# Performance work log

Measured on AMD Instinct MI355X. Metric: run time of the kernel, lower is better.

## Reference

```python
import jax, jax.numpy as jnp
import numpy as np

N_EMBD = 1024
HEAD_SIZE = 128

def setup_inputs() -> dict:
    key = jax.random.key(0)
    k1, k2, k3, k4 = jax.random.split(key, 4)
    x = jax.random.normal(k1, (8, 2048, N_EMBD), dtype=jnp.float32)
    # Linear(n_embd, head_size, bias=False): y = x @ W, W: [n_embd, head_size]
    s = 1.0 / np.sqrt(N_EMBD)
    Wk = jax.random.uniform(k2, (N_EMBD, HEAD_SIZE), jnp.float32, -s, s)
    Wq = jax.random.uniform(k3, (N_EMBD, HEAD_SIZE), jnp.float32, -s, s)
    Wv = jax.random.uniform(k4, (N_EMBD, HEAD_SIZE), jnp.float32, -s, s)
    return {"x": x, "Wk": Wk, "Wq": Wq, "Wv": Wv}

def reference(x, Wk, Wq, Wv):
    B, T, C = x.shape
    H = Wk.shape[1]
    k = jnp.einsum('btc,ch->bth', x, Wk)
    q = jnp.einsum('btc,ch->bth', x, Wq)
    v = jnp.einsum('btc,ch->bth', x, Wv)
    # scores [B, T, T], causal mask, scaled by head_size**-0.5
    wei = jnp.einsum('bqh,bkh->bqk', q, k) * (H ** -0.5)
    causal = jnp.tril(jnp.ones((T, T), dtype=bool))
    wei = jnp.where(causal, wei, -jnp.inf)
    wei = jax.nn.softmax(wei, axis=-1)
    # dropout p=0.0 (eval mode): identity
    out = jnp.einsum('bqk,bkh->bqh', wei, v)
    return out
```

## Files before the change

### kernel.cpp

```cpp
#include <hip/hip_runtime.h>
#include <hip/hip_bf16.h>
#include <stdint.h>

typedef short v8s __attribute__((ext_vector_type(8)));
typedef float v4f __attribute__((ext_vector_type(4)));
typedef float v16f __attribute__((ext_vector_type(16)));

#define N_EMBD 1024
#define HEAD 128
#define TOKENS 16384
#define T_SEQ 2048
#define BATCH 8
#define BPB 96

__device__ __forceinline__ short f2bf(float f) {
    union { float f; uint32_t u; } c; c.f = f;
    uint32_t u = c.u;
    uint32_t r = (u + 0x7fffu + ((u >> 16) & 1u)) >> 16;
    return (short)r;
}

__device__ __forceinline__ float bf2f(short s) {
    union { uint32_t u; float f; } c; c.u = ((uint32_t)(uint16_t)s) << 16;
    return c.f;
}

__global__ __launch_bounds__(256)
void wt_kernel(const float* __restrict__ Wq, const float* __restrict__ Wk,
               const float* __restrict__ Wv, short* __restrict__ wpk) {
    int tid = blockIdx.x * 256 + threadIdx.x;
    int w   = tid >> 17;
    int rem = tid & 131071;
    int c = rem >> 7, h = rem & 127;
    const float* src = (w == 0) ? Wq : ((w == 1) ? Wk : Wv);
    int cb = h >> 5, kb = c >> 4;
    int l  = (h & 31) | (((c >> 3) & 1) << 5);
    wpk[((((w * 4 + cb) * 64) + kb) * 64 + l) * 8 + (c & 7)] = f2bf(src[rem]);
}

__global__ __launch_bounds__(256)
void xpk_kernel(const float* __restrict__ x, short* __restrict__ xpk) {
    const int rb = blockIdx.x >> 1;
    const int kh = blockIdx.x & 1;
    const int t  = threadIdx.x;

    __shared__ short sX[32 * 520];

    for (int it = 0; it < 8; ++it) {
        int idx = it * 256 + t;
        int tok = idx >> 6, ko = idx & 63;
        const float* src = x + (size_t)(rb * 32 + tok) * 1024 + kh * 512 + ko * 8;
        float4 lo = *(const float4*)(src);
        float4 hi = *(const float4*)(src + 4);
        union { short s[8]; uint4 u; } p;
        p.s[0] = f2bf(lo.x); p.s[1] = f2bf(lo.y); p.s[2] = f2bf(lo.z); p.s[3] = f2bf(lo.w);
        p.s[4] = f2bf(hi.x); p.s[5] = f2bf(hi.y); p.s[6] = f2bf(hi.z); p.s[7] = f2bf(hi.w);
        *(uint4*)(&sX[tok * 520 + ko * 8]) = p.u;
    }
    __syncthreads();

    for (int it = 0; it < 8; ++it) {
        int kb_loc = it * 4 + (t >> 6);
        int l = t & 63;
        uint4 d = *(const uint4*)(&sX[(l & 31) * 520 + kb_loc * 16 + (l >> 5) * 8]);
        int kb = kh * 32 + kb_loc;
        *(uint4*)(&xpk[(((size_t)rb * 64 + kb) * 64 + l) * 8]) = d;
    }
}

__global__ __launch_bounds__(256)
void qkv_gemm(const short* __restrict__ xpk, const short* __restrict__ wpk,
              short* __restrict__ qkv, short* __restrict__ vT) {
    const int bid = blockIdx.x;
    const int xcd = bid & 7, q = bid >> 3;
    const int mt  = xcd * 32 + q / 3;
    const int w   = q % 3;
    const int m0  = mt * 64;

    __shared__ short sT[128 * 72];

    const int t = threadIdx.x;
    const int lane = t & 63, wv = t >> 6;
    const int l31 = lane & 31, l1 = lane >> 5;
    const int wm = wv & 1, wn = wv >> 1;

    const int rb = mt * 2 + wm;
    const short* ap  = xpk + (size_t)rb * 32768 + lane * 8;
    const short* bp0 = wpk + (size_t)(w * 4 + 2 * wn) * 32768 + lane * 8;
    const short* bp1 = wpk + (size_t)(w * 4 + 2 * wn + 1) * 32768 + lane * 8;

    v16f acc[2];
    for (int i = 0; i < 16; ++i) { acc[0][i] = 0.f; acc[1][i] = 0.f; }

    v8s A0k0, A0k1, A1k0, A1k1;
    v8s B0k0n0, B0k0n1, B0k1n0, B0k1n1, B1k0n0, B1k0n1, B1k1n0, B1k1n1;

#define LOADSET0(IT) do { int o_ = (IT) * 1024;                                  \
        A0k0   = *(const v8s*)(ap  + o_);                                        \
        A0k1   = *(const v8s*)(ap  + o_ + 512);                                  \
        B0k0n0 = *(const v8s*)(bp0 + o_);                                        \
        B0k0n1 = *(const v8s*)(bp1 + o_);                                        \
        B0k1n0 = *(const v8s*)(bp0 + o_ + 512);                                  \
        B0k1n1 = *(const v8s*)(bp1 + o_ + 512);                                  \
    } while (0)

#define LOADSET1(IT) do { int o_ = (IT) * 1024;                                  \
        A1k0   = *(const v8s*)(ap  + o_);                                        \
        A1k1   = *(const v8s*)(ap  + o_ + 512);                                  \
        B1k0n0 = *(const v8s*)(bp0 + o_);                                        \
        B1k0n1 = *(const v8s*)(bp1 + o_);                                        \
        B1k1n0 = *(const v8s*)(bp0 + o_ + 512);                                  \
        B1k1n1 = *(const v8s*)(bp1 + o_ + 512);                                  \
    } while (0)

#define COMPUTE0() do {                                                          \
        acc[0] = __builtin_amdgcn_mfma_f32_32x32x16_bf16(A0k0, B0k0n0, acc[0], 0, 0, 0); \
        acc[1] = __builtin_amdgcn_mfma_f32_32x32x16_bf16(A0k0, B0k0n1, acc[1], 0, 0, 0); \
        acc[0] = __builtin_amdgcn_mfma_f32_32x32x16_bf16(A0k1, B0k1n0, acc[0], 0, 0, 0); \
        acc[1] = __builtin_amdgcn_mfma_f32_32x32x16_bf16(A0k1, B0k1n1, acc[1], 0, 0, 0); \
    } while (0)

#define COMPUTE1() do {                                                          \
        acc[0] = __builtin_amdgcn_mfma_f32_32x32x16_bf16(A1k0, B1k0n0, acc[0], 0, 0, 0); \
        acc[1] = __builtin_amdgcn_mfma_f32_32x32x16_bf16(A1k0, B1k0n1, acc[1], 0, 0, 0); \
        acc[0] = __builtin_amdgcn_mfma_f32_32x32x16_bf16(A1k1, B1k1n0, acc[0], 0, 0, 0); \
        acc[1] = __builtin_amdgcn_mfma_f32_32x32x16_bf16(A1k1, B1k1n1, acc[1], 0, 0, 0); \
    } while (0)

    LOADSET0(0);
    LOADSET1(1);
    for (int it = 0; it < 32; it += 2) {
        COMPUTE0();
        if (it + 2 < 32) LOADSET0(it + 2);
        COMPUTE1();
        if (it + 3 < 32) LOADSET1(it + 3);
    }

#undef LOADSET0
#undef LOADSET1
#undef COMPUTE0
#undef COMPUTE1

    if (w < 2) {
        short* outw = qkv + (size_t)w * TOKENS * HEAD;
        for (int ni = 0; ni < 2; ++ni) {
            int col = wn * 64 + ni * 32 + l31;
            for (int reg = 0; reg < 16; ++reg) {
                int m = (reg & 3) + 8 * (reg >> 2) + 4 * l1;
                outw[(size_t)(m0 + wm * 32 + m) * HEAD + col] = f2bf(acc[ni][reg]);
            }
        }
    } else {
        __syncthreads();
        for (int ni = 0; ni < 2; ++ni) {
            int col = wn * 64 + ni * 32 + l31;
            for (int g = 0; g < 4; ++g) {
                union { short s[4]; uint64_t u; } pk;
                for (int r = 0; r < 4; ++r) pk.s[r] = f2bf(acc[ni][g * 4 + r]);
                *(uint64_t*)(&sT[col * 72 + wm * 32 + 8 * g + 4 * l1]) = pk.u;
            }
        }
        __syncthreads();
        for (int it = 0; it < 4; ++it) {
            int c = it * 256 + t;
            int col = c >> 3, c8 = c & 7;
            uint4 d = *(const uint4*)(&sT[col * 72 + c8 * 8]);
            *(uint4*)(&vT[(size_t)col * TOKENS + m0 + c8 * 8]) = d;
        }
    }
}

__global__ __launch_bounds__(256)
void attn_kernel(const short* __restrict__ qb, const short* __restrict__ kb,
                 const short* __restrict__ vT, short* __restrict__ po,
                 float* __restrict__ pl) {
    const int bid = blockIdx.x;
    const int b  = bid & 7;
    const int r0 = bid >> 3;
    int qt2 = 0, c0 = 0;
    for (;;) { int sz = (2 * qt2 + 4) / 3; if (r0 < c0 + sz) break; c0 += sz; ++qt2; }
    const int s = r0 - c0;
    const int q0 = qt2 * 128;
    const int nkt = 2 * qt2 + 2;
    const int kt0 = s * 3;
    const int kt1 = (kt0 + 3 < nkt) ? (kt0 + 3) : nkt;

    __shared__ short sK[64 * 128];
    __shared__ short sV[128 * 64];
    __shared__ short sP[128 * 72];

    const int t = threadIdx.x;
    const int wv = t >> 6, lane = t & 63, ln = lane & 15, qd = lane >> 4;
    const int wrow0 = q0 + wv * 32;

    v8s qf[2][4];
    for (int qg = 0; qg < 2; ++qg) {
        const short* qrow = qb + ((size_t)(b * T_SEQ + wrow0 + qg * 16 + ln)) * HEAD;
        for (int ks = 0; ks < 4; ++ks)
            qf[qg][ks] = *(const v8s*)(qrow + ks * 32 + qd * 8);
    }

    v4f o[2][8] = {};
    float rs[2] = {0.f, 0.f};
    const float sc = 1.4426950408889634f / 11.313708498984761f;

    for (int kt = kt0; kt < kt1; ++kt) {
        __syncthreads();
        const short* kbase = kb + ((size_t)(b * T_SEQ + kt * 64)) * HEAD;
        for (int it = 0; it < 4; ++it) {
            int c = it * 256 + t;
            int row = c >> 4, ch = c & 15;
            uint4 d = *(const uint4*)(kbase + row * HEAD + ch * 8);
            int sch = (ch & 8) | ((ch ^ row) & 7);
            *(uint4*)(&sK[row * 128 + sch * 8]) = d;
        }
        const short* vbase = vT + (size_t)(b * T_SEQ + kt * 64);
        for (int it = 0; it < 4; ++it) {
            int c = it * 256 + t;
            int dd = c >> 3, ch = c & 7;
            uint4 d = *(const uint4*)(vbase + (size_t)dd * TOKENS + ch * 8);
            *(uint4*)(&sV[dd * 64 + ((ch ^ dd) & 7) * 8]) = d;
        }
        __syncthreads();

        if (kt * 64 >= wrow0 + 32) continue;

        v4f st[2][4] = {};
        for (int ni = 0; ni < 4; ++ni) {
            int krow = ni * 16 + ln;
            for (int ks = 0; ks < 4; ++ks) {
                int ch = ks * 4 + qd;
                v8s kf = *(const v8s*)&sK[krow * 128 + ((ch & 8) | ((ch ^ krow) & 7)) * 8];
                st[0][ni] = __builtin_amdgcn_mfma_f32_16x16x32_bf16(kf, qf[0][ks], st[0][ni], 0, 0, 0);
                st[1][ni] = __builtin_amdgcn_mfma_f32_16x16x32_bf16(kf, qf[1][ks], st[1][ni], 0, 0, 0);
            }
        }

        const bool needMask = (kt * 64 + 63 > wrow0);
        for (int qg = 0; qg < 2; ++qg) {
            int prow = wv * 32 + qg * 16 + ln;
            int qrow_g = wrow0 + qg * 16 + ln;
            for (int ni = 0; ni < 4; ++ni) {
                union { short s[4]; uint64_t u; } pk;
                for (int r = 0; r < 4; ++r) {
                    float p = exp2f(st[qg][ni][r] * sc);
                    int kg = kt * 64 + ni * 16 + qd * 4 + r;
                    if (needMask && kg > qrow_g) p = 0.f;
                    rs[qg] += p;
                    pk.s[r] = f2bf(p);
                }
                *(uint64_t*)(&sP[prow * 72 + ni * 16 + qd * 4]) = pk.u;
            }
        }

        for (int kk2 = 0; kk2 < 2; ++kk2) {
            v8s pf0 = *(const v8s*)&sP[(wv * 32 + ln) * 72 + kk2 * 32 + qd * 8];
            v8s pf1 = *(const v8s*)&sP[(wv * 32 + 16 + ln) * 72 + kk2 * 32 + qd * 8];
            for (int oni = 0; oni < 8; ++oni) {
                int dd = oni * 16 + ln;
                int ch = kk2 * 4 + qd;
                v8s vf = *(const v8s*)&sV[dd * 64 + ((ch ^ dd) & 7) * 8];
                o[0][oni] = __builtin_amdgcn_mfma_f32_16x16x32_bf16(vf, pf0, o[0][oni], 0, 0, 0);
                o[1][oni] = __builtin_amdgcn_mfma_f32_16x16x32_bf16(vf, pf1, o[1][oni], 0, 0, 0);
            }
        }
    }

    float lsum[2];
    for (int qg = 0; qg < 2; ++qg) {
        float v = rs[qg];
        v += __shfl_xor(v, 16);
        v += __shfl_xor(v, 32);
        lsum[qg] = v;
    }

    short* pob = po + (size_t)bid * 128 * 128;
    for (int qg = 0; qg < 2; ++qg)
        for (int oni = 0; oni < 8; ++oni) {
            union { short s[4]; uint2 u; } pk;
            for (int r = 0; r < 4; ++r) pk.s[r] = f2bf(o[qg][oni][r]);
            *(uint2*)(&pob[(((qg * 8 + oni) * 4 + wv) * 64 + lane) * 4]) = pk.u;
        }
    if (lane < 16)
        for (int qg = 0; qg < 2; ++qg)
            pl[bid * 128 + wv * 32 + qg * 16 + lane] = lsum[qg];
}

__global__ __launch_bounds__(256)
void combine_kernel(const short* __restrict__ po, const float* __restrict__ pl,
                    float* __restrict__ out) {
    const int bid = blockIdx.x;
    const int dh  = bid & 1;
    const int qh  = (bid >> 1) & 1;
    const int qt2 = (bid >> 2) & 15;
    const int b   = bid >> 6;
    int cum = 0;
    for (int j = 0; j < qt2; ++j) cum += (2 * j + 4) / 3;
    const int S = (2 * qt2 + 4) / 3;

    const int t = threadIdx.x;
    const int wv = t >> 6, lane = t & 63, ln = lane & 15, qd = lane >> 4;

    float l = 0.f;
    float accv[4][4] = {};

    for (int si = 0; si < S; ++si) {
        int slot = (cum + si) * 8 + b;
        l += pl[slot * 128 + wv * 32 + qh * 16 + ln];
        const short* pob = po + (size_t)slot * 16384;
        for (int oi = 0; oi < 4; ++oi) {
            int oni = dh * 4 + oi;
            union { short s[4]; uint2 u; } pk;
            pk.u = *(const uint2*)(&pob[(((qh * 8 + oni) * 4 + wv) * 64 + lane) * 4]);
            for (int r = 0; r < 4; ++r) accv[oi][r] += bf2f(pk.s[r]);
        }
    }
    float inv = 1.f / l;
    float* ob = out + ((size_t)(b * T_SEQ) + qt2 * 128 + wv * 32 + qh * 16 + ln) * HEAD;
    for (int oi = 0; oi < 4; ++oi) {
        float4 o4 = make_float4(accv[oi][0] * inv, accv[oi][1] * inv,
                                accv[oi][2] * inv, accv[oi][3] * inv);
        *(float4*)(ob + (dh * 4 + oi) * 16 + qd * 4) = o4;
    }
}

extern "C" void kernel_launch(void* const* d_in, const int* in_sizes, int n_in,
                              void* d_out, int out_size, void* d_ws, size_t ws_size,
                              hipStream_t stream) {
    const float* x  = (const float*)d_in[0];
    const float* Wk = (const float*)d_in[1];
    const float* Wq = (const float*)d_in[2];
    const float* Wv = (const float*)d_in[3];
    float* out = (float*)d_out;

    char* ws = (char*)d_ws;
    short* wpk = (short*)ws;
    short* xpk = (short*)(ws + 0x100000u);
    short* qb  = (short*)(ws + 0x2100000u);
    short* kb  = (short*)(ws + 0x2500000u);
    short* vT  = (short*)(ws + 0x2900000u);
    short* po  = (short*)ws;
    float* pl  = (float*)(ws + 0x1800000u);
    short* qkv = qb;

    wt_kernel<<<1536, 256, 0, stream>>>(Wq, Wk, Wv, wpk);
    xpk_kernel<<<1024, 256, 0, stream>>>(x, xpk);
    qkv_gemm<<<768, 256, 0, stream>>>(xpk, wpk, qkv, vT);
    attn_kernel<<<BATCH * BPB, 256, 0, stream>>>(qb, kb, vT, po, pl);
    combine_kernel<<<512, 256, 0, stream>>>(po, pl, out);
}
```

Before: 166.5 us.

## Pre-pack K and V into MFMA fragment layout and read directly from global

The QKV GEMM epilogue now writes K and V tiles already arranged in the per-lane MFMA operand layout, staging them through shared memory. The attention kernel then drops its shared-memory staging of K and V and its two block barriers per key tile, loading operand fragments straight from global memory with coalesced 16-byte loads. It also exits the key loop early once tiles are fully masked. The trade-off is that each of the four waves reloads the same K/V fragments from global/L2, with no LDS reuse, so latency is exposed without explicit prefetch.

```diff
diff --git a/kernel.cpp b/kernel.cpp
--- a/kernel.cpp
+++ b/kernel.cpp
@@ -70,7 +70,8 @@
 
 __global__ __launch_bounds__(256)
 void qkv_gemm(const short* __restrict__ xpk, const short* __restrict__ wpk,
-              short* __restrict__ qkv, short* __restrict__ vT) {
+              short* __restrict__ qkv, short* __restrict__ kpk,
+              short* __restrict__ vpk) {
     const int bid = blockIdx.x;
     const int xcd = bid & 7, q = bid >> 3;
     const int mt  = xcd * 32 + q / 3;
@@ -141,17 +142,34 @@
 #undef COMPUTE0
 #undef COMPUTE1
 
-    if (w < 2) {
-        short* outw = qkv + (size_t)w * TOKENS * HEAD;
+    const int b_  = m0 >> 11;
+    const int kt_ = (m0 >> 6) & 31;
+    if (w == 0) {
         for (int ni = 0; ni < 2; ++ni) {
             int col = wn * 64 + ni * 32 + l31;
             for (int reg = 0; reg < 16; ++reg) {
                 int m = (reg & 3) + 8 * (reg >> 2) + 4 * l1;
-                outw[(size_t)(m0 + wm * 32 + m) * HEAD + col] = f2bf(acc[ni][reg]);
+                qkv[(size_t)(m0 + wm * 32 + m) * HEAD + col] = f2bf(acc[ni][reg]);
             }
         }
+    } else if (w == 1) {
+        for (int ni = 0; ni < 2; ++ni) {
+            int col = wn * 64 + ni * 32 + l31;
+            for (int reg = 0; reg < 16; ++reg) {
+                int m = (reg & 3) + 8 * (reg >> 2) + 4 * l1;
+                sT[(wm * 32 + m) * 136 + col] = f2bf(acc[ni][reg]);
+            }
+        }
+        __syncthreads();
+        short* kdst = kpk + ((size_t)(b_ * 32 + kt_) * 16) * 512;
+        for (int it = 0; it < 4; ++it) {
+            int c = it * 256 + t;
+            int chunk = c >> 6, l = c & 63;
+            int ni2 = chunk >> 2, ks = chunk & 3;
+            uint4 d = *(const uint4*)(&sT[(ni2 * 16 + (l & 15)) * 136 + ks * 32 + (l >> 4) * 8]);
+            *(uint4*)(&kdst[chunk * 512 + l * 8]) = d;
+        }
     } else {
-        __syncthreads();
         for (int ni = 0; ni < 2; ++ni) {
             int col = wn * 64 + ni * 32 + l31;
             for (int g = 0; g < 4; ++g) {
@@ -161,18 +179,20 @@
             }
         }
         __syncthreads();
+        short* vdst = vpk + ((size_t)(b_ * 32 + kt_) * 16) * 512;
         for (int it = 0; it < 4; ++it) {
             int c = it * 256 + t;
-            int col = c >> 3, c8 = c & 7;
-            uint4 d = *(const uint4*)(&sT[col * 72 + c8 * 8]);
-            *(uint4*)(&vT[(size_t)col * TOKENS + m0 + c8 * 8]) = d;
-        }
-    }
-}
-
-__global__ __launch_bounds__(256)
-void attn_kernel(const short* __restrict__ qb, const short* __restrict__ kb,
-                 const short* __restrict__ vT, short* __restrict__ po,
+            int chunk = c >> 6, l = c & 63;
+            int oni = chunk >> 1, kk2 = chunk & 1;
+            uint4 d = *(const uint4*)(&sT[(oni * 16 + (l & 15)) * 72 + kk2 * 32 + (l >> 4) * 8]);
+            *(uint4*)(&vdst[chunk * 512 + l * 8]) = d;
+        }
+    }
+}
+
+__global__ __launch_bounds__(256)
+void attn_kernel(const short* __restrict__ qb, const short* __restrict__ kpk,
+                 const short* __restrict__ vpk, short* __restrict__ po,
                  float* __restrict__ pl) {
     const int bid = blockIdx.x;
     const int b  = bid & 7;
@@ -185,8 +205,6 @@
     const int kt0 = s * 3;
     const int kt1 = (kt0 + 3 < nkt) ? (kt0 + 3) : nkt;
 
-    __shared__ short sK[64 * 128];
-    __shared__ short sV[128 * 64];
     __shared__ short sP[128 * 72];
 
     const int t = threadIdx.x;
@@ -204,36 +222,29 @@
     float rs[2] = {0.f, 0.f};
     const float sc = 1.4426950408889634f / 11.313708498984761f;
 
+    const short* kbB = kpk + ((size_t)b * 32 * 16) * 512 + lane * 8;
+    const short* vbB = vpk + ((size_t)b * 32 * 16) * 512 + lane * 8;
+
     for (int kt = kt0; kt < kt1; ++kt) {
-        __syncthreads();
-        const short* kbase = kb + ((size_t)(b * T_SEQ + kt * 64)) * HEAD;
-        for (int it = 0; it < 4; ++it) {
-            int c = it * 256 + t;
-            int row = c >> 4, ch = c & 15;
-            uint4 d = *(const uint4*)(kbase + row * HEAD + ch * 8);
-            int sch = (ch & 8) | ((ch ^ row) & 7);
-            *(uint4*)(&sK[row * 128 + sch * 8]) = d;
-        }
-        const short* vbase = vT + (size_t)(b * T_SEQ + kt * 64);
-        for (int it = 0; it < 4; ++it) {
-            int c = it * 256 + t;
-            int dd = c >> 3, ch = c & 7;
-            uint4 d = *(const uint4*)(vbase + (size_t)dd * TOKENS + ch * 8);
-            *(uint4*)(&sV[dd * 64 + ((ch ^ dd) & 7) * 8]) = d;
-        }
-        __syncthreads();
-
-        if (kt * 64 >= wrow0 + 32) continue;
+        if (kt * 64 >= wrow0 + 32) break;
+        const short* kc = kbB + (size_t)kt * 8192;
+        const short* vc = vbB + (size_t)kt * 8192;
 
         v4f st[2][4] = {};
+#pragma unroll
         for (int ni = 0; ni < 4; ++ni) {
-            int krow = ni * 16 + ln;
-            for (int ks = 0; ks < 4; ++ks) {
-                int ch = ks * 4 + qd;
-                v8s kf = *(const v8s*)&sK[krow * 128 + ((ch & 8) | ((ch ^ krow) & 7)) * 8];
-                st[0][ni] = __builtin_amdgcn_mfma_f32_16x16x32_bf16(kf, qf[0][ks], st[0][ni], 0, 0, 0);
-                st[1][ni] = __builtin_amdgcn_mfma_f32_16x16x32_bf16(kf, qf[1][ks], st[1][ni], 0, 0, 0);
-            }
+            v8s kf0 = *(const v8s*)(kc + (ni * 4 + 0) * 512);
+            v8s kf1 = *(const v8s*)(kc + (ni * 4 + 1) * 512);
+            v8s kf2 = *(const v8s*)(kc + (ni * 4 + 2) * 512);
+            v8s kf3 = *(const v8s*)(kc + (ni * 4 + 3) * 512);
+            st[0][ni] = __builtin_amdgcn_mfma_f32_16x16x32_bf16(kf0, qf[0][0], st[0][ni], 0, 0, 0);
+            st[1][ni] = __builtin_amdgcn_mfma_f32_16x16x32_bf16(kf0, qf[1][0], st[1][ni], 0, 0, 0);
+            st[0][ni] = __builtin_amdgcn_mfma_f32_16x16x32_bf16(kf1, qf[0][1], st[0][ni], 0, 0, 0);
+            st[1][ni] = __builtin_amdgcn_mfma_f32_16x16x32_bf16(kf1, qf[1][1], st[1][ni], 0, 0, 0);
+            st[0][ni] = __builtin_amdgcn_mfma_f32_16x16x32_bf16(kf2, qf[0][2], st[0][ni], 0, 0, 0);
+            st[1][ni] = __builtin_amdgcn_mfma_f32_16x16x32_bf16(kf2, qf[1][2], st[1][ni], 0, 0, 0);
+            st[0][ni] = __builtin_amdgcn_mfma_f32_16x16x32_bf16(kf3, qf[0][3], st[0][ni], 0, 0, 0);
+            st[1][ni] = __builtin_amdgcn_mfma_f32_16x16x32_bf16(kf3, qf[1][3], st[1][ni], 0, 0, 0);
         }
 
         const bool needMask = (kt * 64 + 63 > wrow0);
@@ -253,16 +264,27 @@
             }
         }
 
-        for (int kk2 = 0; kk2 < 2; ++kk2) {
-            v8s pf0 = *(const v8s*)&sP[(wv * 32 + ln) * 72 + kk2 * 32 + qd * 8];
-            v8s pf1 = *(const v8s*)&sP[(wv * 32 + 16 + ln) * 72 + kk2 * 32 + qd * 8];
-            for (int oni = 0; oni < 8; ++oni) {
-                int dd = oni * 16 + ln;
-                int ch = kk2 * 4 + qd;
-                v8s vf = *(const v8s*)&sV[dd * 64 + ((ch ^ dd) & 7) * 8];
-                o[0][oni] = __builtin_amdgcn_mfma_f32_16x16x32_bf16(vf, pf0, o[0][oni], 0, 0, 0);
-                o[1][oni] = __builtin_amdgcn_mfma_f32_16x16x32_bf16(vf, pf1, o[1][oni], 0, 0, 0);
-            }
+        v8s pf[2][2];
+#pragma unroll
+        for (int qg = 0; qg < 2; ++qg)
+#pragma unroll
+            for (int kk2 = 0; kk2 < 2; ++kk2)
+                pf[qg][kk2] = *(const v8s*)&sP[(wv * 32 + qg * 16 + ln) * 72 + kk2 * 32 + qd * 8];
+
+#pragma unroll
+        for (int og = 0; og < 4; ++og) {
+            v8s vf00 = *(const v8s*)(vc + ((og * 2 + 0) * 2 + 0) * 512);
+            v8s vf01 = *(const v8s*)(vc + ((og * 2 + 0) * 2 + 1) * 512);
+            v8s vf10 = *(const v8s*)(vc + ((og * 2 + 1) * 2 + 0) * 512);
+            v8s vf11 = *(const v8s*)(vc + ((og * 2 + 1) * 2 + 1) * 512);
+            o[0][og * 2]     = __builtin_amdgcn_mfma_f32_16x16x32_bf16(vf00, pf[0][0], o[0][og * 2], 0, 0, 0);
+            o[0][og * 2]     = __builtin_amdgcn_mfma_f32_16x16x32_bf16(vf01, pf[0][1], o[0][og * 2], 0, 0, 0);
+            o[1][og * 2]     = __builtin_amdgcn_mfma_f32_16x16x32_bf16(vf00, pf[1][0], o[1][og * 2], 0, 0, 0);
+            o[1][og * 2]     = __builtin_amdgcn_mfma_f32_16x16x32_bf16(vf01, pf[1][1], o[1][og * 2], 0, 0, 0);
+            o[0][og * 2 + 1] = __builtin_amdgcn_mfma_f32_16x16x32_bf16(vf10, pf[0][0], o[0][og * 2 + 1], 0, 0, 0);
+            o[0][og * 2 + 1] = __builtin_amdgcn_mfma_f32_16x16x32_bf16(vf11, pf[0][1], o[0][og * 2 + 1], 0, 0, 0);
+            o[1][og * 2 + 1] = __builtin_amdgcn_mfma_f32_16x16x32_bf16(vf10, pf[1][0], o[1][og * 2 + 1], 0, 0, 0);
+            o[1][og * 2 + 1] = __builtin_amdgcn_mfma_f32_16x16x32_bf16(vf11, pf[1][1], o[1][og * 2 + 1], 0, 0, 0);
         }
     }
 
@@ -337,15 +359,15 @@
     short* wpk = (short*)ws;
     short* xpk = (short*)(ws + 0x100000u);
     short* qb  = (short*)(ws + 0x2100000u);
-    short* kb  = (short*)(ws + 0x2500000u);
-    short* vT  = (short*)(ws + 0x2900000u);
+    short* kpk = (short*)(ws + 0x2500000u);
+    short* vpk = (short*)(ws + 0x2900000u);
     short* po  = (short*)ws;
     float* pl  = (float*)(ws + 0x1800000u);
     short* qkv = qb;
 
     wt_kernel<<<1536, 256, 0, stream>>>(Wq, Wk, Wv, wpk);
     xpk_kernel<<<1024, 256, 0, stream>>>(x, xpk);
-    qkv_gemm<<<768, 256, 0, stream>>>(xpk, wpk, qkv, vT);
-    attn_kernel<<<BATCH * BPB, 256, 0, stream>>>(qb, kb, vT, po, pl);
+    qkv_gemm<<<768, 256, 0, stream>>>(xpk, wpk, qkv, kpk, vpk);
+    attn_kernel<<<BATCH * BPB, 256, 0, stream>>>(qb, kpk, vpk, po, pl);
     combine_kernel<<<512, 256, 0, stream>>>(po, pl, out);
 }
```

Result: no change. 166.4 us (-0.0%).
